# Kernel optimization log

Measured on AMD Instinct MI355X. Metric: run time of the kernel, lower is better.

## Reference

```python
import jax, jax.numpy as jnp
import numpy as np

NUM_CLASSES = 21
THRESH = 0.5
NEG_POS = 3
VAR0, VAR1 = 0.1, 0.2  # SSD cfg['variance']
B, P, O = 32, 32768, 50


def point_form(boxes):
    # center form (cx,cy,w,h) -> corner form (xmin,ymin,xmax,ymax)
    return jnp.concatenate([boxes[:, :2] - boxes[:, 2:] / 2,
                            boxes[:, :2] + boxes[:, 2:] / 2], axis=1)


def jaccard(box_a, box_b):
    # box_a [A,4], box_b [B,4], corner form -> IoU [A,B]
    max_xy = jnp.minimum(box_a[:, None, 2:], box_b[None, :, 2:])
    min_xy = jnp.maximum(box_a[:, None, :2], box_b[None, :, :2])
    inter = jnp.prod(jnp.clip(max_xy - min_xy, 0.0, None), axis=2)
    area_a = jnp.prod(box_a[:, 2:] - box_a[:, :2], axis=1)[:, None]
    area_b = jnp.prod(box_b[:, 2:] - box_b[:, :2], axis=1)[None, :]
    return inter / (area_a + area_b - inter)


def encode(matched, priors):
    # matched corner form [P,4], priors center form [P,4]
    g_cxcy = ((matched[:, :2] + matched[:, 2:]) / 2 - priors[:, :2]) / (VAR0 * priors[:, 2:])
    g_wh = jnp.log((matched[:, 2:] - matched[:, :2]) / priors[:, 2:]) / VAR1
    return jnp.concatenate([g_cxcy, g_wh], axis=1)


def match_one(truths, labels, priors):
    # truths [O,4] corner, labels [O], priors [P,4] center
    overlaps = jaccard(truths, point_form(priors))          # [O,P]
    best_prior_idx = jnp.argmax(overlaps, axis=1)           # [O]
    best_truth_overlap = jnp.max(overlaps, axis=0)          # [P]
    best_truth_idx = jnp.argmax(overlaps, axis=0)           # [P]
    # ensure every gt matches its best prior
    best_truth_overlap = best_truth_overlap.at[best_prior_idx].set(2.0)
    best_truth_idx = best_truth_idx.at[best_prior_idx].set(jnp.arange(truths.shape[0]))
    matches = truths[best_truth_idx]                        # [P,4]
    conf = (labels[best_truth_idx] + 1.0).astype(jnp.int32)
    conf = jnp.where(best_truth_overlap < THRESH, 0, conf)
    return encode(matches, priors), conf


def setup_inputs() -> dict:
    key = jax.random.key(0)
    k1, k2, k3, k4, k5, k6 = jax.random.split(key, 6)
    loc_data = jax.random.normal(k1, (B, P, 4), dtype=jnp.float32)
    conf_data = jax.random.normal(k2, (B, P, NUM_CLASSES), dtype=jnp.float32)
    # priors in center form: centers in (0,1), sizes in (0.02, 0.5)
    cxy = jax.random.uniform(k3, (P, 2), dtype=jnp.float32)
    wh = jax.random.uniform(k4, (P, 2), dtype=jnp.float32, minval=0.02, maxval=0.5)
    priors = jnp.concatenate([cxy, wh], axis=1)
    # targets: valid corner-form boxes + label
    pts = jax.random.uniform(k5, (B, O, 2, 2), dtype=jnp.float32)
    xymin = pts.min(axis=2)
    xymax = jnp.maximum(pts.max(axis=2), xymin + 0.01)
    labels = jax.random.randint(k6, (B, O), 0, NUM_CLASSES - 1).astype(jnp.float32)
    targets = jnp.concatenate([xymin, xymax, labels[..., None]], axis=-1)
    return {"loc_data": loc_data, "conf_data": conf_data, "priors": priors, "targets": targets}


def reference(loc_data, conf_data, priors, targets):
    truths = targets[..., :4]
    labels = targets[..., 4]
    loc_t, conf_t = jax.vmap(match_one, in_axes=(0, 0, None))(truths, labels, priors)
    loc_t = jax.lax.stop_gradient(loc_t)
    conf_t = jax.lax.stop_gradient(conf_t)

    pos = conf_t > 0                                         # [B,P]
    # localization: smooth-L1, summed over positives
    diff = loc_data - loc_t
    ad = jnp.abs(diff)
    sl1 = jnp.where(ad < 1.0, 0.5 * diff * diff, ad - 0.5)
    loss_l = jnp.sum(sl1 * pos[..., None].astype(sl1.dtype))

    # per-prior softmax CE (logsumexp - true logit)
    lse = jax.nn.logsumexp(conf_data, axis=-1)               # [B,P]
    true_logit = jnp.take_along_axis(conf_data, conf_t[..., None], axis=-1)[..., 0]
    ce = lse - true_logit                                    # [B,P]

    # hard negative mining: rank negatives by CE (pos zeroed out)
    ce_mine = jnp.where(pos, 0.0, ce)
    loss_idx = jnp.argsort(-ce_mine, axis=1)
    idx_rank = jnp.argsort(loss_idx, axis=1)
    num_pos = jnp.sum(pos, axis=1, keepdims=True)            # [B,1]
    num_neg = jnp.clip(NEG_POS * num_pos, None, pos.shape[1] - 1)
    neg = idx_rank < num_neg

    sel = pos | neg
    loss_c = jnp.sum(jnp.where(sel, ce, 0.0))

    N = jnp.sum(num_pos).astype(loss_l.dtype)
    return loss_l / N, loss_c / N
```

## Files before the change

### kernel.cpp

```cpp
#include <hip/hip_runtime.h>
#include <math.h>

#define BB 32
#define PP 32768
#define OO 50
#define NT 25
#define NC 21

#define WBINLO (104 << 7)
#define WBINS  2048

typedef unsigned long long u64;
typedef unsigned int u32;

static constexpr u32 HALF_BITS = 0x3F000000u;

static constexpr size_t OFF_WHC   = 0;
static constexpr size_t OFF_WHS   = OFF_WHC  + 4ull*BB*WBINS;
static constexpr size_t OFF_NPOS  = OFF_WHS  + 4ull*BB*WBINS;
static constexpr size_t OFF_DACC  = OFF_NPOS + 128;
static constexpr size_t OFF_DONE  = OFF_DACC + 8ull*3*BB;
static constexpr size_t ZERO_BYTES = OFF_DONE + 16;
static constexpr size_t OFF_KPART = ((ZERO_BYTES + 127) & ~127ull);
static constexpr size_t OFF_KEY2  = OFF_KPART + 8ull*BB*OO*64;

static __device__ __forceinline__ float fast_div(float a, float b) {
    return a * __builtin_amdgcn_rcpf(b);
}
static __device__ __forceinline__ u32 top16bits(float v) {
    u32 u = __float_as_uint(v);
    return (v > 0.0f) ? u : 0u;
}
static __device__ __forceinline__ u64 umax64(u64 a, u64 b) { return a > b ? a : b; }
static __device__ __forceinline__ u32 umax32(u32 a, u32 b) { return a > b ? a : b; }

__global__ __launch_bounds__(256) void match_kernel(
    const float* __restrict__ priors, const float* __restrict__ targets,
    u32* __restrict__ key2, u64* __restrict__ kpart, ulonglong2* __restrict__ zbase)
{
    const int b = blockIdx.y;
    const int half = blockIdx.z;
    const int obase = half * NT;
    const int tid = threadIdx.x;
    const int lane = tid & 63, wid = tid >> 6;
    const int chunk = blockIdx.x;
    const int p = chunk * 1024 + tid * 4;

    if (b == 0 && half == 0) {
        for (size_t i = (size_t)chunk * 256 + tid; i < ZERO_BYTES / 16; i += 32 * 256)
            zbase[i] = make_ulonglong2(0ull, 0ull);
    }

    __shared__ float tr[NT * 5];
    __shared__ u64 wkeys[4][NT];
    if (tid < NT * 5) tr[tid] = targets[(size_t)b * OO * 5 + obase * 5 + tid];
    __syncthreads();

    float px1[4], py1[4], px2[4], py2[4], area_p[4];
#pragma unroll
    for (int s = 0; s < 4; ++s) {
        float4 pr = *(const float4*)(priors + (size_t)(p + s) * 4);
        px1[s] = pr.x - pr.z * 0.5f; py1[s] = pr.y - pr.w * 0.5f;
        px2[s] = pr.x + pr.z * 0.5f; py2[s] = pr.y + pr.w * 0.5f;
        area_p[s] = (px2[s] - px1[s]) * (py2[s] - py1[s]);
    }

    float bestv[4]; int besto[4];
#pragma unroll
    for (int s = 0; s < 4; ++s) { bestv[s] = -1.0f; besto[s] = 0; }

    for (int o = 0; o < NT; ++o) {
        float tx1 = tr[o*5+0], ty1 = tr[o*5+1], tx2 = tr[o*5+2], ty2 = tr[o*5+3];
        float area_t = (tx2 - tx1) * (ty2 - ty1);
        float iou[4];
#pragma unroll
        for (int s = 0; s < 4; ++s) {
            float ix1 = fmaxf(tx1, px1[s]), iy1 = fmaxf(ty1, py1[s]);
            float ix2 = fminf(tx2, px2[s]), iy2 = fminf(ty2, py2[s]);
            float dx = fmaxf(ix2 - ix1, 0.0f), dy = fmaxf(iy2 - iy1, 0.0f);
            float inter = dx * dy;
            iou[s] = fast_div(inter, (area_t + area_p[s]) - inter);
            if (iou[s] > bestv[s]) { bestv[s] = iou[s]; besto[s] = o; }
        }
        float tmax = iou[0]; int ts = 0;
#pragma unroll
        for (int s = 1; s < 4; ++s) if (iou[s] > tmax) { tmax = iou[s]; ts = s; }
        float mv = tmax;
        for (int m = 1; m < 64; m <<= 1)
            mv = fmaxf(mv, __shfl_xor(mv, m, 64));
        u64 bm = __ballot(tmax == mv);
        if (lane == (int)(__ffsll((long long)bm) - 1))
            wkeys[wid][o] = ((u64)__float_as_uint(mv) << 32)
                          | (u64)(0xFFFFFFFFu - (u32)(p + ts));
    }

    {
        uint4 kv;
        kv.x = (__float_as_uint(bestv[0]) & ~63u) | (u32)(49 - (obase + besto[0]));
        kv.y = (__float_as_uint(bestv[1]) & ~63u) | (u32)(49 - (obase + besto[1]));
        kv.z = (__float_as_uint(bestv[2]) & ~63u) | (u32)(49 - (obase + besto[2]));
        kv.w = (__float_as_uint(bestv[3]) & ~63u) | (u32)(49 - (obase + besto[3]));
        *(uint4*)(key2 + ((size_t)half * BB + b) * PP + p) = kv;
    }
    __syncthreads();
    if (tid < NT) {
        u64 k0 = wkeys[0][tid];
#pragma unroll
        for (int w = 1; w < 4; ++w) k0 = umax64(k0, wkeys[w][tid]);
        kpart[((size_t)b * OO + obase + tid) * 64 + chunk * 2 + half] = k0;
    }
}

#define EL2(k) ((((k) & 1) == 0) ? v[(k) >> 1].x : v[(k) >> 1].y)

__global__ __launch_bounds__(256) void score_kernel(
    const float* __restrict__ loc, const float* __restrict__ conf,
    const float* __restrict__ priors, const float* __restrict__ targets,
    const u32* __restrict__ key2, const u64* __restrict__ kpart,
    int* __restrict__ npos, double* __restrict__ dacc,
    u32* __restrict__ whc, float* __restrict__ whs)
{
    const int b = blockIdx.y;
    const int tid = threadIdx.x;
    const int p = blockIdx.x * 512 + tid * 2;
    __shared__ float tr[OO * 5];
    __shared__ u32 fp[OO];
    __shared__ __align__(16) u32 hh[WBINS];
    __shared__ __align__(16) float hs[WBINS];
    if (tid < OO * 5) tr[tid] = targets[(size_t)b * OO * 5 + tid];
    if (tid < OO) {
        const u64* kp = kpart + ((size_t)b * OO + tid) * 64;
        u64 k0 = kp[0];
        for (int c = 1; c < 64; ++c) k0 = umax64(k0, kp[c]);
        fp[tid] = 0xFFFFFFFFu - (u32)(k0 & 0xFFFFFFFFull);
    }
#pragma unroll
    for (int j = 0; j < WBINS / 256; ++j) { hh[j * 256 + tid] = 0; hs[j * 256 + tid] = 0.0f; }
    __syncthreads();

    uint2 a01 = *(const uint2*)(key2 + (size_t)b * PP + p);
    uint2 c01 = *(const uint2*)(key2 + ((size_t)BB + b) * PP + p);
    const u32 kk[2] = {umax32(a01.x, c01.x), umax32(a01.y, c01.y)};

    int fo[2] = {-1, -1};
    for (int o = 0; o < OO; ++o) {
        u32 fpo = fp[o];
#pragma unroll
        for (int r = 0; r < 2; ++r) if (fpo == (u32)(p + r)) fo[r] = o;
    }

    const float2* cp = (const float2*)(conf + (size_t)((size_t)b * PP + p) * NC);
    float2 v[21];
#pragma unroll
    for (int j = 0; j < 21; ++j) v[j] = cp[j];

    float cev[2];
    double l_l = 0.0, pce = 0.0; int np_ = 0;

#pragma unroll
    for (int r = 0; r < 2; ++r) {
        const bool forced = fo[r] >= 0;
        const int o = forced ? fo[r] : (int)(49u - (kk[r] & 63u));
        const bool pos = forced || kk[r] >= HALF_BITS;
        const int conft = pos ? (int)(tr[o * 5 + 4] + 1.0f) : 0;

        float m = -1e30f;
#pragma unroll
        for (int c = 0; c < NC; ++c) m = fmaxf(m, EL2(21 * r + c));
        float s = 0.0f, tl = 0.0f;
#pragma unroll
        for (int c = 0; c < NC; ++c) {
            float xx = EL2(21 * r + c);
            s += expf(xx - m);
            if (c == conft) tl = xx;
        }
        float ce = (m + logf(s)) - tl;
        cev[r] = pos ? 0.0f : ce;

        if (pos) {
            np_ += 1; pce += (double)ce;
            float mx1 = tr[o*5+0], my1 = tr[o*5+1], mx2 = tr[o*5+2], my2 = tr[o*5+3];
            float4 pr = *(const float4*)(priors + (size_t)(p + r) * 4);
            float lt0 = ((mx1 + mx2) * 0.5f - pr.x) / (0.1f * pr.z);
            float lt1 = ((my1 + my2) * 0.5f - pr.y) / (0.1f * pr.w);
            float lt2 = logf((mx2 - mx1) / pr.z) / 0.2f;
            float lt3 = logf((my2 - my1) / pr.w) / 0.2f;
            float4 l4 = *(const float4*)(loc + (size_t)((size_t)b * PP + p + r) * 4);
            float lpv[4] = {l4.x, l4.y, l4.z, l4.w};
            float lt[4] = {lt0, lt1, lt2, lt3};
#pragma unroll
            for (int i2 = 0; i2 < 4; ++i2) {
                float d = lpv[i2] - lt[i2];
                float ad = fabsf(d);
                l_l += (double)(ad < 1.0f ? 0.5f * d * d : ad - 0.5f);
            }
        }
    }

#pragma unroll
    for (int r = 0; r < 2; ++r) {
        u32 t16 = top16bits(cev[r]) >> 16;
        if (t16 != 0) {
            int widx = ((int)t16 - WBINLO) >> 1;
            widx = widx < 0 ? 0 : (widx > WBINS - 1 ? WBINS - 1 : widx);
            atomicAdd(&hh[widx], 1u);
            atomicAdd(&hs[widx], cev[r]);
        }
    }
    __syncthreads();
#pragma unroll
    for (int j = 0; j < WBINS / 256; ++j) {
        u32 c = hh[j * 256 + tid];
        if (c) {
            atomicAdd(&whc[(size_t)b * WBINS + j * 256 + tid], c);
            atomicAdd(&whs[(size_t)b * WBINS + j * 256 + tid], hs[j * 256 + tid]);
        }
    }
    __syncthreads();
    double* rl = (double*)hh;
    double* rc = (double*)hs;
    int*    rn = (int*)(hh + 1024);
    rl[tid] = l_l; rc[tid] = pce; rn[tid] = np_;
    __syncthreads();
    for (int s2 = 128; s2 > 0; s2 >>= 1) {
        if (tid < s2) { rl[tid] += rl[tid+s2]; rc[tid] += rc[tid+s2]; rn[tid] += rn[tid+s2]; }
        __syncthreads();
    }
    if (tid == 0) {
        atomicAdd(&dacc[b], rl[0]);
        atomicAdd(&dacc[BB + b], rc[0]);
        atomicAdd(&npos[b], rn[0]);
    }
}

__global__ __launch_bounds__(256) void selwin_kernel(
    const u32* __restrict__ whc, const float* __restrict__ whs,
    const int* __restrict__ npos, double* __restrict__ dacc,
    u32* __restrict__ done, float* __restrict__ out)
{
    const int b = blockIdx.x, tid = threadIdx.x;
    const int lane = tid & 63, wid = tid >> 6;
    int k = npos[b] * 3; if (k > PP - 1) k = PP - 1;

    __shared__ u32 ccnt_[WBINS / 256]; __shared__ float csum_[WBINS / 256];
    __shared__ u32 ct[256]; __shared__ float fs[256];
    __shared__ int s_cT; __shared__ u32 s_aboveC; __shared__ float s_aboveS;
    __shared__ u32 sT;

    if (k > 0) {
        const u32* hc = whc + (size_t)b * WBINS;
        const float* hsg = whs + (size_t)b * WBINS;
        for (int c = wid; c < WBINS / 256; c += 4) {
            u32 cnt = 0; float sm = 0.0f;
#pragma unroll
            for (int q = 0; q < 4; ++q) {
                int idx = c * 256 + q * 64 + lane;
                cnt += hc[idx];
                sm  += hsg[idx];
            }
            for (int m = 1; m < 64; m <<= 1) {
                cnt += __shfl_xor(cnt, m, 64);
                sm  += __shfl_xor(sm, m, 64);
            }
            if (lane == 0) { ccnt_[c] = cnt; csum_[c] = sm; }
        }
        if (tid == 0) sT = 0;
        __syncthreads();
        if (tid == 0) {
            u32 cum = 0; float scum = 0.0f; int cT = -1; u32 aC = 0; float aS = 0.0f;
            for (int c = WBINS / 256 - 1; c >= 0; --c) {
                if (cum + ccnt_[c] >= (u32)k) { cT = c; aC = cum; aS = scum; break; }
                cum += ccnt_[c]; scum += csum_[c];
            }
            s_cT = cT; s_aboveC = aC; s_aboveS = aS;
            if (cT < 0) { dacc[2 * BB + b] = (double)scum; __threadfence(); }
        }
        __syncthreads();
        const int cT = s_cT;
        if (cT >= 0) {
            const u32 aboveC = s_aboveC; const float aboveS = s_aboveS;
            const u32 myc = hc[cT * 256 + tid];
            const float mys = hsg[cT * 256 + tid];
            ct[tid] = myc; fs[tid] = mys;
            __syncthreads();
            for (int off = 1; off < 256; off <<= 1) {
                u32 a1 = (tid + off < 256) ? ct[tid + off] : 0;
                float a2 = (tid + off < 256) ? fs[tid + off] : 0.0f;
                __syncthreads();
                ct[tid] += a1; fs[tid] += a2;
                __syncthreads();
            }
            if (aboveC + ct[tid] >= (u32)k) atomicMax(&sT, (u32)tid);
            __syncthreads();
            const int T = (int)sT;
            if (tid == T) {
                u32 aboveBinC = aboveC + ((T < 255) ? ct[T + 1] : 0);
                float aboveBinS = aboveS + ((T < 255) ? fs[T + 1] : 0.0f);
                int k2 = k - (int)aboveBinC;
                double avg = (double)mys / (double)myc;
                dacc[2 * BB + b] = (double)aboveBinS + (double)k2 * avg;
                __threadfence();
            }
        }
    }
    __syncthreads();
    if (tid == 0) {
        u32 d = atomicAdd(done, 1u);
        if (d == BB - 1) {
            __threadfence();
            double N = 0.0, ll = 0.0, lc = 0.0;
            for (int bb = 0; bb < BB; ++bb) {
                N += (double)npos[bb];
                ll += dacc[bb];
                lc += dacc[BB + bb] + dacc[2 * BB + bb];
            }
            out[0] = (float)(ll / N);
            out[1] = (float)(lc / N);
        }
    }
}

extern "C" void kernel_launch(void* const* d_in, const int* in_sizes, int n_in,
                              void* d_out, int out_size, void* d_ws, size_t ws_size,
                              hipStream_t stream) {
    const float* loc     = (const float*)d_in[0];
    const float* conf    = (const float*)d_in[1];
    const float* priors  = (const float*)d_in[2];
    const float* targets = (const float*)d_in[3];
    char* ws = (char*)d_ws;
    u32*    whc   = (u32*)   (ws + OFF_WHC);
    float*  whs   = (float*) (ws + OFF_WHS);
    int*    npos  = (int*)   (ws + OFF_NPOS);
    double* dacc  = (double*)(ws + OFF_DACC);
    u32*    done  = (u32*)   (ws + OFF_DONE);
    u64*    kpart = (u64*)   (ws + OFF_KPART);
    u32*    key2  = (u32*)   (ws + OFF_KEY2);
    float*  out   = (float*)d_out;

    match_kernel<<<dim3(PP / 1024, BB, 2), 256, 0, stream>>>(priors, targets, key2, kpart, (ulonglong2*)ws);
    score_kernel<<<dim3(PP / 512, BB), 256, 0, stream>>>(loc, conf, priors, targets, key2, kpart, npos, dacc, whc, whs);
    selwin_kernel<<<BB, 256, 0, stream>>>(whc, whs, npos, dacc, done, out);
}
```

Baseline: 92.59 us.

## Fuse selection-window kernel into score kernel via last-block-per-batch counter

Removes the separate selwin_kernel launch. Each score block bumps a per-batch atomic counter, and the last of the 64 blocks for a batch does the histogram threshold search and the partial-sum accumulation. A second global counter then picks the final block to write the output. This cuts one kernel launch and its inter-kernel gap, at the cost of extra fences and atomics in every score block.

After: 281.2 us. 204% more time.

```diff
diff --git a/kernel.cpp b/kernel.cpp
--- a/kernel.cpp
+++ b/kernel.cpp
@@ -19,8 +19,9 @@
 static constexpr size_t OFF_WHS   = OFF_WHC  + 4ull*BB*WBINS;
 static constexpr size_t OFF_NPOS  = OFF_WHS  + 4ull*BB*WBINS;
 static constexpr size_t OFF_DACC  = OFF_NPOS + 128;
-static constexpr size_t OFF_DONE  = OFF_DACC + 8ull*3*BB;
-static constexpr size_t ZERO_BYTES = OFF_DONE + 16;
+static constexpr size_t OFF_DONEB = OFF_DACC + 8ull*3*BB;
+static constexpr size_t OFF_DONE2 = OFF_DONEB + 128;
+static constexpr size_t ZERO_BYTES = OFF_DONE2 + 16;
 static constexpr size_t OFF_KPART = ((ZERO_BYTES + 127) & ~127ull);
 static constexpr size_t OFF_KEY2  = OFF_KPART + 8ull*BB*OO*64;
 
@@ -118,10 +119,12 @@
     const float* __restrict__ priors, const float* __restrict__ targets,
     const u32* __restrict__ key2, const u64* __restrict__ kpart,
     int* __restrict__ npos, double* __restrict__ dacc,
-    u32* __restrict__ whc, float* __restrict__ whs)
+    u32* __restrict__ whc, float* __restrict__ whs,
+    u32* __restrict__ doneb, u32* __restrict__ done2, float* __restrict__ out)
 {
     const int b = blockIdx.y;
     const int tid = threadIdx.x;
+    const int lane = tid & 63, wid = tid >> 6;
     const int p = blockIdx.x * 512 + tid * 2;
     __shared__ float tr[OO * 5];
     __shared__ u32 fp[OO];
@@ -217,33 +220,33 @@
         }
     }
     __syncthreads();
-    double* rl = (double*)hh;
-    double* rc = (double*)hs;
-    int*    rn = (int*)(hh + 1024);
-    rl[tid] = l_l; rc[tid] = pce; rn[tid] = np_;
-    __syncthreads();
-    for (int s2 = 128; s2 > 0; s2 >>= 1) {
-        if (tid < s2) { rl[tid] += rl[tid+s2]; rc[tid] += rc[tid+s2]; rn[tid] += rn[tid+s2]; }
+    {
+        double* rl = (double*)hh;
+        double* rc = (double*)hs;
+        int*    rn = (int*)(hh + 1024);
+        rl[tid] = l_l; rc[tid] = pce; rn[tid] = np_;
         __syncthreads();
-    }
-    if (tid == 0) {
-        atomicAdd(&dacc[b], rl[0]);
-        atomicAdd(&dacc[BB + b], rc[0]);
-        atomicAdd(&npos[b], rn[0]);
-    }
-}
-
-__global__ __launch_bounds__(256) void selwin_kernel(
-    const u32* __restrict__ whc, const float* __restrict__ whs,
-    const int* __restrict__ npos, double* __restrict__ dacc,
-    u32* __restrict__ done, float* __restrict__ out)
-{
-    const int b = blockIdx.x, tid = threadIdx.x;
-    const int lane = tid & 63, wid = tid >> 6;
+        for (int s2 = 128; s2 > 0; s2 >>= 1) {
+            if (tid < s2) { rl[tid] += rl[tid+s2]; rc[tid] += rc[tid+s2]; rn[tid] += rn[tid+s2]; }
+            __syncthreads();
+        }
+        if (tid == 0) {
+            atomicAdd(&dacc[b], rl[0]);
+            atomicAdd(&dacc[BB + b], rc[0]);
+            atomicAdd(&npos[b], rn[0]);
+        }
+    }
+
+    __threadfence();
+    __shared__ u32 s_rank;
+    if (tid == 0) s_rank = atomicAdd(&doneb[b], 1u);
+    __syncthreads();
+    if (s_rank != 63u) return;
+    __threadfence();
+
     int k = npos[b] * 3; if (k > PP - 1) k = PP - 1;
-
+    u32* ct = hh; float* fs = hs;
     __shared__ u32 ccnt_[WBINS / 256]; __shared__ float csum_[WBINS / 256];
-    __shared__ u32 ct[256]; __shared__ float fs[256];
     __shared__ int s_cT; __shared__ u32 s_aboveC; __shared__ float s_aboveS;
     __shared__ u32 sT;
 
@@ -273,14 +276,14 @@
                 cum += ccnt_[c]; scum += csum_[c];
             }
             s_cT = cT; s_aboveC = aC; s_aboveS = aS;
-            if (cT < 0) { dacc[2 * BB + b] = (double)scum; __threadfence(); }
+            if (cT < 0) dacc[2 * BB + b] = (double)scum;
         }
         __syncthreads();
         const int cT = s_cT;
         if (cT >= 0) {
             const u32 aboveC = s_aboveC; const float aboveS = s_aboveS;
-            const u32 myc = hc[cT * 256 + tid];
-            const float mys = hsg[cT * 256 + tid];
+            const u32 myc = (whc + (size_t)b * WBINS)[cT * 256 + tid];
+            const float mys = (whs + (size_t)b * WBINS)[cT * 256 + tid];
             ct[tid] = myc; fs[tid] = mys;
             __syncthreads();
             for (int off = 1; off < 256; off <<= 1) {
@@ -299,13 +302,13 @@
                 int k2 = k - (int)aboveBinC;
                 double avg = (double)mys / (double)myc;
                 dacc[2 * BB + b] = (double)aboveBinS + (double)k2 * avg;
-                __threadfence();
-            }
-        }
-    }
+            }
+        }
+    }
+    __threadfence();
     __syncthreads();
     if (tid == 0) {
-        u32 d = atomicAdd(done, 1u);
+        u32 d = atomicAdd(done2, 1u);
         if (d == BB - 1) {
             __threadfence();
             double N = 0.0, ll = 0.0, lc = 0.0;
@@ -332,12 +335,13 @@
     float*  whs   = (float*) (ws + OFF_WHS);
     int*    npos  = (int*)   (ws + OFF_NPOS);
     double* dacc  = (double*)(ws + OFF_DACC);
-    u32*    done  = (u32*)   (ws + OFF_DONE);
+    u32*    doneb = (u32*)   (ws + OFF_DONEB);
+    u32*    done2 = (u32*)   (ws + OFF_DONE2);
     u64*    kpart = (u64*)   (ws + OFF_KPART);
     u32*    key2  = (u32*)   (ws + OFF_KEY2);
     float*  out   = (float*)d_out;
 
     match_kernel<<<dim3(PP / 1024, BB, 2), 256, 0, stream>>>(priors, targets, key2, kpart, (ulonglong2*)ws);
-    score_kernel<<<dim3(PP / 512, BB), 256, 0, stream>>>(loc, conf, priors, targets, key2, kpart, npos, dacc, whc, whs);
-    selwin_kernel<<<BB, 256, 0, stream>>>(whc, whs, npos, dacc, done, out);
-}
+    score_kernel<<<dim3(PP / 512, BB), 256, 0, stream>>>(loc, conf, priors, targets, key2, kpart,
+                                                         npos, dacc, whc, whs, doneb, done2, out);
+}
```
